# Kernel optimization log

Hardware: AMD Instinct MI355X
Metric: run time of the kernel (lower is better)

Reference implementation:

```python
import jax, jax.numpy as jnp
import numpy as np

EMBED_DIM = 128
NUM_HEADS = 16
HEAD_DIM = EMBED_DIM // NUM_HEADS
SCALE = HEAD_DIM ** -0.5


def setup_inputs() -> dict:
    key = jax.random.key(0)
    ks = jax.random.split(key, 9)
    B, S, E = 4, 2048, EMBED_DIM
    s = 1.0 / np.sqrt(E)
    return {
        "x": jax.random.normal(ks[0], (B, S, E), dtype=jnp.float32),
        "Wq": jax.random.uniform(ks[1], (E, E), jnp.float32, -s, s),
        "bq": jax.random.uniform(ks[2], (E,), jnp.float32, -s, s),
        "Wk": jax.random.uniform(ks[3], (E, E), jnp.float32, -s, s),
        "bk": jax.random.uniform(ks[4], (E,), jnp.float32, -s, s),
        "Wv": jax.random.uniform(ks[5], (E, E), jnp.float32, -s, s),
        "bv": jax.random.uniform(ks[6], (E,), jnp.float32, -s, s),
        "Wo": jax.random.uniform(ks[7], (E, E), jnp.float32, -s, s),
        "bo": jax.random.uniform(ks[8], (E,), jnp.float32, -s, s),
    }


def reference(x, Wq, bq, Wk, bk, Wv, bv, Wo, bo):
    B, S, E = x.shape
    H, D = NUM_HEADS, HEAD_DIM
    # projections (torch Linear: x @ W.T + b)
    q = (x @ Wq.T + bq).reshape(B, S, H, D).transpose(0, 2, 1, 3)  # [B,H,S,D]
    k = (x @ Wk.T + bk).reshape(B, S, H, D).transpose(0, 2, 1, 3)
    v = (x @ Wv.T + bv).reshape(B, S, H, D).transpose(0, 2, 1, 3)
    scores = jnp.einsum("bhqd,bhkd->bhqk", q, k) * SCALE  # [B,H,S,S]
    causal_mask = jnp.triu(jnp.ones((S, S), dtype=bool), k=1)  # True above diag
    scores = jnp.where(causal_mask, jnp.float32(-1e9), scores)
    w = jax.nn.sigmoid(scores)
    w = w / jnp.sum(w, axis=-1, keepdims=True)  # sigmoid-sum normalization
    attn = jnp.einsum("bhqk,bhkd->bhqd", w, v)  # [B,H,S,D]
    attn = attn.transpose(0, 2, 1, 3).reshape(B, S, E)
    return attn @ Wo.T + bo
```

## Files before the change

### kernel.cpp

```cpp
#include <hip/hip_runtime.h>
#include <math.h>

#define EDIM 128
#define NHEAD 16
#define HDIM 8
#define SEQ 2048
#define BATCH 4
#define NROW (BATCH*SEQ)
#define QNEG (-0.35355339059327373f * 1.4426950408889634f)

#if __has_builtin(__builtin_amdgcn_exp2f)
#define EXP2F(x) __builtin_amdgcn_exp2f(x)
#else
#define EXP2F(x) exp2f(x)
#endif
#define RCPF(x) __builtin_amdgcn_rcpf(x)

typedef __attribute__((ext_vector_type(8))) short short8v;
typedef __attribute__((ext_vector_type(4))) short short4v;
typedef __attribute__((ext_vector_type(4))) float float4v;
typedef __attribute__((ext_vector_type(16))) float float16v;

union U16x8 { uint4 u; short8v s; };
union U16x4 { uint2 u; short4v s; };

#define MFMA32(a,b,c) __builtin_amdgcn_mfma_f32_32x32x16_bf16(a,b,c,0,0,0)

__device__ __forceinline__ void lane32swap(unsigned &x, unsigned &y) {
#if __has_builtin(__builtin_amdgcn_permlane32_swap)
  typedef __attribute__((ext_vector_type(2))) unsigned uint2v;
  uint2v r = __builtin_amdgcn_permlane32_swap(x, y, false, false);
  x = r[0]; y = r[1];
#else
  asm volatile("v_permlane32_swap_b32 %0, %1" : "+v"(x), "+v"(y));
#endif
}

__device__ __forceinline__ unsigned pk_bf16(float a, float b) {
  unsigned ua = __float_as_uint(a), ub = __float_as_uint(b);
  unsigned lo = (ua + 0x7fffu + ((ua >> 16) & 1u)) >> 16;
  unsigned hi = (ub + 0x7fffu + ((ub >> 16) & 1u)) & 0xffff0000u;
  return lo | hi;
}

__device__ __forceinline__ float16v zero16() {
  float16v z;
  #pragma unroll
  for (int i = 0; i < 16; ++i) z[i] = 0.f;
  return z;
}

__device__ __forceinline__
void afrags(const unsigned short* xs, int lq, int qd, short8v a[4])
{
  #pragma unroll
  for (int kk = 0; kk < 4; ++kk) {
    const unsigned addr =
        (unsigned)(lq * 256 + kk * 64 + qd * 16) ^ (unsigned)((lq & 7) << 4);
    a[kk] = *(const short8v*)((const char*)xs + addr);
  }
}

template<int MODE>
__device__ __forceinline__
void proj32(const float* __restrict__ X, const float* __restrict__ W,
            const float* __restrict__ bias, void* __restrict__ out,
            int row0, int tid,
            unsigned short* wlds, unsigned short* xs, unsigned short* bnc)
{
  {
    const int n = tid >> 1, h = (tid & 1) * 64;
    const float4* src = (const float4*)(W + (size_t)n * EDIM + h);
    const unsigned xr = (unsigned)((n & 7) << 4);
    #pragma unroll
    for (int j = 0; j < 8; ++j) {
      const float4 f0 = src[2 * j], f1 = src[2 * j + 1];
      const uint4 v = make_uint4(pk_bf16(f0.x, f0.y), pk_bf16(f0.z, f0.w),
                                 pk_bf16(f1.x, f1.y), pk_bf16(f1.z, f1.w));
      *(uint4*)((char*)wlds + ((unsigned)(n * 256 + h * 2 + j * 16) ^ xr)) = v;
    }
  }
  {
    const int r = tid >> 3, c = tid & 7;
    const float4* src = (const float4*)(X + (size_t)(row0 + r) * EDIM + c * 16);
    const unsigned xr = (unsigned)((r & 7) << 4);
    const float4 f0 = src[0], f1 = src[1], f2 = src[2], f3 = src[3];
    const uint4 v0 = make_uint4(pk_bf16(f0.x, f0.y), pk_bf16(f0.z, f0.w),
                                pk_bf16(f1.x, f1.y), pk_bf16(f1.z, f1.w));
    const uint4 v1 = make_uint4(pk_bf16(f2.x, f2.y), pk_bf16(f2.z, f2.w),
                                pk_bf16(f3.x, f3.y), pk_bf16(f3.z, f3.w));
    *(uint4*)((char*)xs + ((unsigned)(r * 256 + c * 32) ^ xr)) = v0;
    *(uint4*)((char*)xs + ((unsigned)(r * 256 + c * 32 + 16) ^ xr)) = v1;
  }
  __syncthreads();

  const int lane = tid & 63, wv = tid >> 6;
  const int lq = lane & 15, qd = lane >> 4;
  const int n0 = wv * 32;

  short8v b0[4], b1[4];
  #pragma unroll
  for (int kk = 0; kk < 4; ++kk) {
    const unsigned ad = (unsigned)((n0 + lq) * 256 + kk * 64 + qd * 16)
                      ^ (unsigned)((lq & 7) << 4);
    b0[kk] = *(const short8v*)((const char*)wlds + ad);
    b1[kk] = *(const short8v*)((const char*)wlds + ad + 4096);
  }

  const int nA = n0 + lq, nB = nA + 16;
  const float bzA = bias[nA], bzB = bias[nB];
  const int b_ = row0 >> 11;

  #pragma unroll
  for (int rt = 0; rt < 2; ++rt) {
    const int rowt = row0 + rt * 16;
    short8v a[4];
    afrags(xs + rt * 2048, lq, qd, a);

    float4v D0 = {0.f, 0.f, 0.f, 0.f}, D1 = {0.f, 0.f, 0.f, 0.f};
    #pragma unroll
    for (int kk = 0; kk < 4; ++kk) {
      D0 = __builtin_amdgcn_mfma_f32_16x16x32_bf16(a[kk], b0[kk], D0, 0, 0, 0);
      D1 = __builtin_amdgcn_mfma_f32_16x16x32_bf16(a[kk], b1[kk], D1, 0, 0, 0);
    }

    if (MODE == 3) {
      float* of = (float*)out + (size_t)(rowt + qd * 4) * EDIM + nA;
      #pragma unroll
      for (int r = 0; r < 4; ++r) {
        of[r * EDIM]      = D0[r] + bzA;
        of[r * EDIM + 16] = D1[r] + bzB;
      }
      continue;
    }

    const int srel = rowt & (SEQ - 1);

    if (MODE == 2) {
      const int tg = srel >> 4;
      unsigned short* oU = (unsigned short*)out;
      {
        const int bh = b_ * NHEAD + (nA >> 3), dv = nA & 7;
        uint2 p;
        p.x = pk_bf16(D0[0] + bzA, D0[1] + bzA);
        p.y = pk_bf16(D0[2] + bzA, D0[3] + bzA);
        *(uint2*)(oU + (size_t)bh * (SEQ * HDIM) + tg * 128 + dv * 16 + qd * 4) = p;
      }
      {
        const int bh = b_ * NHEAD + (nB >> 3), dv = nB & 7;
        uint2 p;
        p.x = pk_bf16(D1[0] + bzB, D1[1] + bzB);
        p.y = pk_bf16(D1[2] + bzB, D1[3] + bzB);
        *(uint2*)(oU + (size_t)bh * (SEQ * HDIM) + tg * 128 + dv * 16 + qd * 4) = p;
      }
      continue;
    }

    #pragma unroll
    for (int r = 0; r < 4; ++r) {
      float vA = D0[r] + bzA, vB = D1[r] + bzB;
      if (MODE == 0) { vA *= QNEG; vB *= QNEG; }
      const int m = qd * 4 + r;
      bnc[m * 20 + lq]       = (unsigned short)pk_bf16(vA, 0.f);
      bnc[320 + m * 20 + lq] = (unsigned short)pk_bf16(vB, 0.f);
    }
    __syncthreads();

    const int mm   = lane & 15;
    const int half = (lane >> 4) & 1;
    const int tile = lane >> 5;
    const unsigned short* sp = bnc + tile * 320 + mm * 20 + half * 8;
    const uint2 w0 = *(const uint2*)sp;
    const uint2 w1 = *(const uint2*)(sp + 4);
    const int bh = b_ * NHEAD + wv * 4 + tile * 2 + half;
    unsigned short* dp = (unsigned short*)out + ((size_t)bh * SEQ + srel + mm) * 8;
    *(uint4*)dp = make_uint4(w0.x, w0.y, w1.x, w1.y);
    __syncthreads();
  }
}

__global__ __launch_bounds__(256)
void qkv_kernel(const float* __restrict__ X,
                const float* __restrict__ Wq, const float* __restrict__ Wk,
                const float* __restrict__ Wv,
                const float* __restrict__ bq, const float* __restrict__ bk,
                const float* __restrict__ bv,
                unsigned* __restrict__ qb, unsigned* __restrict__ kb,
                unsigned* __restrict__ vb)
{
  __shared__ __align__(16) unsigned short wlds[16384];
  __shared__ __align__(16) unsigned short xs[4096];
  __shared__ __align__(16) unsigned short bnc[4 * 640];
  const int tid = threadIdx.x;
  const int row0 = blockIdx.x * 32;
  unsigned short* myb = bnc + (tid >> 6) * 640;
  const int m = blockIdx.y;
  if (m == 0)      proj32<0>(X, Wq, bq, (void*)qb, row0, tid, wlds, xs, myb);
  else if (m == 1) proj32<1>(X, Wk, bk, (void*)kb, row0, tid, wlds, xs, myb);
  else             proj32<2>(X, Wv, bv, (void*)vb, row0, tid, wlds, xs, myb);
}

__global__ __launch_bounds__(256)
void oproj_kernel(const float* __restrict__ A, const float* __restrict__ Wo,
                  const float* __restrict__ bo, float* __restrict__ out)
{
  __shared__ __align__(16) unsigned short wlds[16384];
  __shared__ __align__(16) unsigned short xs[4096];
  proj32<3>(A, Wo, bo, (void*)out, blockIdx.x * 32, threadIdx.x, wlds, xs, nullptr);
}

template<bool DIAG>
__device__ __forceinline__
float16v step32(const uint4* __restrict__ Kg,
                const unsigned short* __restrict__ Vtbh,
                int t, U16x8 qf, float16v acc,
                int lane, unsigned voff, bool is8)
{
  U16x8 kf; kf.u = Kg[32 * t + (lane & 31)];
  const unsigned short* vt = Vtbh + 256 * t;
  U16x8 v1, v2;
  {
    const uint4 a = *(const uint4*)(vt + voff);
    const uint4 b = *(const uint4*)(vt + 128 + voff);
    const uint4 ones = make_uint4(0x3F803F80u, 0x3F803F80u,
                                  0x3F803F80u, 0x3F803F80u);
    v1.u = is8 ? ones : a;
    v2.u = is8 ? ones : b;
  }

  float16v st = MFMA32(kf.s, qf.s, zero16());

  unsigned u[8];
  #pragma unroll
  for (int i = 0; i < 8; ++i) {
    float s0 = RCPF(1.f + EXP2F(st[2 * i]));
    float s1 = RCPF(1.f + EXP2F(st[2 * i + 1]));
    if (DIAG) {
      const int rb = ((2 * i) & 3) + 8 * (i >> 1) + ((lane >> 5) << 2);
      const int q_ = lane & 31;
      s0 = (rb     <= q_) ? s0 : 0.f;
      s1 = (rb + 1 <= q_) ? s1 : 0.f;
    }
    const unsigned b0 = __float_as_uint(s0) + 0x8000u;
    const unsigned b1 = __float_as_uint(s1) + 0x8000u;
    u[i] = __builtin_amdgcn_perm(b1, b0, 0x07060302u);
  }

  lane32swap(u[0], u[2]);
  lane32swap(u[1], u[3]);
  lane32swap(u[4], u[6]);
  lane32swap(u[5], u[7]);

  U16x8 pa, pb;
  pa.u = make_uint4(u[0], u[1], u[2], u[3]);
  pb.u = make_uint4(u[4], u[5], u[6], u[7]);
  acc = MFMA32(pa.s, v1.s, acc);
  acc = MFMA32(pb.s, v2.s, acc);
  return acc;
}

__device__ __forceinline__
void seg32(const uint4* __restrict__ Kg, const unsigned short* __restrict__ Vtbh,
           U16x8 qf, int T, int a, int b, float16v &acc,
           int lane, unsigned voff, bool is8)
{
  if (a >= b) return;
  const bool hasDiag = (b == T + 1);
  const int e = hasDiag ? b - 1 : b;
  for (int t = a; t < e; ++t)
    acc = step32<false>(Kg, Vtbh, t, qf, acc, lane, voff, is8);
  if (hasDiag)
    acc = step32<true>(Kg, Vtbh, T, qf, acc, lane, voff, is8);
}

__device__ __forceinline__
void epilogue32(float16v acc, int T, int bh, int lane, float* __restrict__ out)
{
  const int b_ = bh >> 4, h = bh & 15;
  const int n = lane & 31;
  const int pidx = ((lane & 32) | 8) << 2;
  const int rowb = 32 * T + ((lane >> 5) << 2);
  #pragma unroll
  for (int reg = 0; reg < 16; ++reg) {
    const float den = __int_as_float(
        __builtin_amdgcn_ds_bpermute(pidx, __float_as_int(acc[reg])));
    const float val = acc[reg] * RCPF(den);
    const int row = rowb + (reg & 3) + 8 * (reg >> 2);
    if (n < 8)
      out[(size_t)(b_ * SEQ + row) * EDIM + h * HDIM + n] = val;
  }
}

__global__ __launch_bounds__(128, 4)
void attn_kernel(const unsigned* __restrict__ Qb, const unsigned* __restrict__ Kb,
                 const unsigned* __restrict__ Vb, float* __restrict__ out)
{
  __shared__ float cmb[2][64][16];

  const int bh   = blockIdx.x & 63;
  const int g    = blockIdx.x >> 6;
  const int w    = threadIdx.x >> 6;
  const int lane = threadIdx.x & 63;
  const int L = g, H = 63 - g;

  const uint4* Kg = (const uint4*)Kb + (size_t)bh * 2048;
  const uint4* Qg = (const uint4*)Qb + (size_t)bh * 2048;
  const unsigned short* Vtbh = (const unsigned short*)Vb + (size_t)bh * SEQ * HDIM;

  const unsigned voff = (unsigned)((lane & 7) * 16 + ((lane >> 5) << 3));
  const bool is8 = (lane & 31) == 8;

  U16x8 qfl, qfh;
  {
    const uint4 zz = make_uint4(0u, 0u, 0u, 0u);
    qfl.u = (lane < 32) ? Qg[32 * L + lane] : zz;
    qfh.u = (lane < 32) ? Qg[32 * H + lane] : zz;
  }

  float16v accL = zero16();
  float16v accH = zero16();

  const int st_ = w ? 32 : 0;
  const int en_ = w ? 65 : 32;
  const int Lp1 = L + 1;
  const int aL = (st_ < Lp1) ? st_ : Lp1;
  const int bL = (en_ < Lp1) ? en_ : Lp1;
  int aH = st_ - Lp1; if (aH < 0) aH = 0;
  int bH = en_ - Lp1; if (bH > H + 1) bH = H + 1;

  seg32(Kg, Vtbh, qfl, L, aL, bL, accL, lane, voff, is8);
  seg32(Kg, Vtbh, qfh, H, aH, bH, accH, lane, voff, is8);

  if (w == 1) {
    #pragma unroll
    for (int i = 0; i < 4; ++i) {
      *(float4*)&cmb[0][lane][4 * i] =
          make_float4(accL[4*i], accL[4*i+1], accL[4*i+2], accL[4*i+3]);
      *(float4*)&cmb[1][lane][4 * i] =
          make_float4(accH[4*i], accH[4*i+1], accH[4*i+2], accH[4*i+3]);
    }
  }
  __syncthreads();

  if (w == 0) {
    #pragma unroll
    for (int i = 0; i < 16; ++i) {
      accL[i] += cmb[0][lane][i];
      accH[i] += cmb[1][lane][i];
    }
    epilogue32(accL, L, bh, lane, out);
    epilogue32(accH, H, bh, lane, out);
  }
}

extern "C" void kernel_launch(void* const* d_in, const int* in_sizes, int n_in,
                              void* d_out, int out_size, void* d_ws, size_t ws_size,
                              hipStream_t stream)
{
  const float* x  = (const float*)d_in[0];
  const float* Wq = (const float*)d_in[1];
  const float* bq = (const float*)d_in[2];
  const float* Wk = (const float*)d_in[3];
  const float* bk = (const float*)d_in[4];
  const float* Wv = (const float*)d_in[5];
  const float* bv = (const float*)d_in[6];
  const float* Wo = (const float*)d_in[7];
  const float* bo = (const float*)d_in[8];

  float* ws = (float*)d_ws;
  float*    attn = ws + 65536;
  unsigned* Qb   = (unsigned*)(ws + 65536 + 1048576);
  unsigned* Kb   = Qb + (size_t)524288;
  unsigned* Vb   = Kb + (size_t)524288;

  qkv_kernel<<<dim3(NROW / 32, 3), 256, 0, stream>>>(x, Wq, Wk, Wv, bq, bk, bv,
                                                     Qb, Kb, Vb);
  attn_kernel<<<dim3(2048), 128, 0, stream>>>(Qb, Kb, Vb, attn);
  oproj_kernel<<<dim3(NROW / 32), 256, 0, stream>>>(attn, Wo, bo, (float*)d_out);
}
```

Before: 124.4 us.

## Split attention KV range across four waves and prefetch next K/V tile

The attention block grows from two to four wavefronts. Each wave takes roughly a quarter of the 65 key tiles for the paired query tiles, and the partial accumulators are combined through a two-level LDS tree reduction with padded rows. The inner loop now loads the next tile's K and V into registers before computing the current tile, so load latency is hidden. This adds more parallelism per block and latency overlap, at the cost of extra syncthreads, extra LDS traffic, and more register pressure, which may limit occupancy.

```diff
diff --git a/kernel.cpp b/kernel.cpp
--- a/kernel.cpp
+++ b/kernel.cpp
@@ -211,21 +211,15 @@
 
 template<bool DIAG>
 __device__ __forceinline__
-float16v step32(const uint4* __restrict__ Kg,
-                const unsigned short* __restrict__ Vtbh,
-                int t, U16x8 qf, float16v acc,
-                int lane, unsigned voff, bool is8)
-{
-  U16x8 kf; kf.u = Kg[32 * t + (lane & 31)];
-  const unsigned short* vt = Vtbh + 256 * t;
+float16v compute32(U16x8 kf, uint4 va, uint4 vb, U16x8 qf, float16v acc,
+                   int lane, bool is8)
+{
   U16x8 v1, v2;
   {
-    const uint4 a = *(const uint4*)(vt + voff);
-    const uint4 b = *(const uint4*)(vt + 128 + voff);
     const uint4 ones = make_uint4(0x3F803F80u, 0x3F803F80u,
                                   0x3F803F80u, 0x3F803F80u);
-    v1.u = is8 ? ones : a;
-    v2.u = is8 ? ones : b;
+    v1.u = is8 ? ones : va;
+    v2.u = is8 ? ones : vb;
   }
 
   float16v st = MFMA32(kf.s, qf.s, zero16());
@@ -265,12 +259,23 @@
            int lane, unsigned voff, bool is8)
 {
   if (a >= b) return;
+  const int l31 = lane & 31;
   const bool hasDiag = (b == T + 1);
-  const int e = hasDiag ? b - 1 : b;
-  for (int t = a; t < e; ++t)
-    acc = step32<false>(Kg, Vtbh, t, qf, acc, lane, voff, is8);
-  if (hasDiag)
-    acc = step32<true>(Kg, Vtbh, T, qf, acc, lane, voff, is8);
+  const int last = b - 1;
+
+  U16x8 kf; kf.u = Kg[32 * a + l31];
+  uint4 va = *(const uint4*)(Vtbh + 256 * a + voff);
+  uint4 vb = *(const uint4*)(Vtbh + 256 * a + 128 + voff);
+
+  for (int t = a; t < last; ++t) {
+    U16x8 kn; kn.u = Kg[32 * (t + 1) + l31];
+    const uint4 vna = *(const uint4*)(Vtbh + 256 * (t + 1) + voff);
+    const uint4 vnb = *(const uint4*)(Vtbh + 256 * (t + 1) + 128 + voff);
+    acc = compute32<false>(kf, va, vb, qf, acc, lane, is8);
+    kf = kn; va = vna; vb = vnb;
+  }
+  if (hasDiag) acc = compute32<true >(kf, va, vb, qf, acc, lane, is8);
+  else         acc = compute32<false>(kf, va, vb, qf, acc, lane, is8);
 }
 
 __device__ __forceinline__
@@ -291,11 +296,22 @@
   }
 }
 
-__global__ __launch_bounds__(128, 4)
+__device__ __forceinline__
+void cmb_store(float* slot, int lane, float16v v) {
+  #pragma unroll
+  for (int i = 0; i < 16; ++i) slot[lane * 17 + i] = v[i];
+}
+__device__ __forceinline__
+void cmb_add(float* slot, int lane, float16v &v) {
+  #pragma unroll
+  for (int i = 0; i < 16; ++i) v[i] += slot[lane * 17 + i];
+}
+
+__global__ __launch_bounds__(256, 4)
 void attn_kernel(const unsigned* __restrict__ Qb, const unsigned* __restrict__ Kb,
                  const unsigned* __restrict__ Vb, float* __restrict__ out)
 {
-  __shared__ float cmb[2][64][16];
+  __shared__ float cmb[2][2][64 * 17];
 
   const int bh   = blockIdx.x & 63;
   const int g    = blockIdx.x >> 6;
@@ -320,8 +336,8 @@
   float16v accL = zero16();
   float16v accH = zero16();
 
-  const int st_ = w ? 32 : 0;
-  const int en_ = w ? 65 : 32;
+  const int st_ = (w == 0) ? 0 : (w == 1) ? 17 : (w == 2) ? 33 : 49;
+  const int en_ = (w == 0) ? 17 : (w == 1) ? 33 : (w == 2) ? 49 : 65;
   const int Lp1 = L + 1;
   const int aL = (st_ < Lp1) ? st_ : Lp1;
   const int bL = (en_ < Lp1) ? en_ : Lp1;
@@ -331,23 +347,17 @@
   seg32(Kg, Vtbh, qfl, L, aL, bL, accL, lane, voff, is8);
   seg32(Kg, Vtbh, qfh, H, aH, bH, accH, lane, voff, is8);
 
-  if (w == 1) {
-    #pragma unroll
-    for (int i = 0; i < 4; ++i) {
-      *(float4*)&cmb[0][lane][4 * i] =
-          make_float4(accL[4*i], accL[4*i+1], accL[4*i+2], accL[4*i+3]);
-      *(float4*)&cmb[1][lane][4 * i] =
-          make_float4(accH[4*i], accH[4*i+1], accH[4*i+2], accH[4*i+3]);
-    }
-  }
+  if (w == 1) { cmb_store(cmb[0][0], lane, accL); cmb_store(cmb[0][1], lane, accH); }
+  if (w == 3) { cmb_store(cmb[1][0], lane, accL); cmb_store(cmb[1][1], lane, accH); }
   __syncthreads();
-
+  if (w == 0) { cmb_add(cmb[0][0], lane, accL); cmb_add(cmb[0][1], lane, accH); }
+  if (w == 2) { cmb_add(cmb[1][0], lane, accL); cmb_add(cmb[1][1], lane, accH); }
+  __syncthreads();
+  if (w == 2) { cmb_store(cmb[0][0], lane, accL); cmb_store(cmb[0][1], lane, accH); }
+  __syncthreads();
   if (w == 0) {
-    #pragma unroll
-    for (int i = 0; i < 16; ++i) {
-      accL[i] += cmb[0][lane][i];
-      accH[i] += cmb[1][lane][i];
-    }
+    cmb_add(cmb[0][0], lane, accL);
+    cmb_add(cmb[0][1], lane, accH);
     epilogue32(accL, L, bh, lane, out);
     epilogue32(accH, H, bh, lane, out);
   }
@@ -375,6 +385,6 @@
 
   qkv_kernel<<<dim3(NROW / 32, 3), 256, 0, stream>>>(x, Wq, Wk, Wv, bq, bk, bv,
                                                      Qb, Kb, Vb);
-  attn_kernel<<<dim3(2048), 128, 0, stream>>>(Qb, Kb, Vb, attn);
+  attn_kernel<<<dim3(2048), 256, 0, stream>>>(Qb, Kb, Vb, attn);
   oproj_kernel<<<dim3(NROW / 32), 256, 0, stream>>>(attn, Wo, bo, (float*)d_out);
 }
```

Measured after the change: 123.7 us. About the same (-0.5%).
